# Optimization experiments

Measured on AMD Instinct MI355X. Metric: run time of the kernel, lower is better.

Reference implementation:

```python
import jax, jax.numpy as jnp
import numpy as np

NO, NR, E, D = 50000, 2000, 600000, 128
NEG_SLOPE = 0.2


def setup_inputs() -> dict:
    key = jax.random.key(0)
    ks = jax.random.split(key, 16)
    p = lambda k, shape: jax.random.normal(k, shape, dtype=jnp.float32) * 0.05
    return {
        "x_order": jax.random.normal(ks[0], (NO, D), dtype=jnp.float32),
        "x_rider": jax.random.normal(ks[1], (NR, D), dtype=jnp.float32),
        "order_idx": jax.random.randint(ks[2], (E,), 0, NO),
        "rider_idx": jax.random.randint(ks[3], (E,), 0, NR),
        # GATConv layer 1 (order_input_dim=128 -> hidden_dim=128, heads=1)
        "Ws1": p(ks[4], (D, D)), "Wd1": p(ks[5], (D, D)),
        "as1": p(ks[6], (D,)), "ad1": p(ks[7], (D,)), "b1": jnp.zeros((D,), jnp.float32),
        # GATConv layer 2 (hidden_dim=128 -> output_dim=128, heads=1)
        "Ws2": p(ks[8], (D, D)), "Wd2": p(ks[9], (D, D)),
        "as2": p(ks[10], (D,)), "ad2": p(ks[11], (D,)), "b2": jnp.zeros((D,), jnp.float32),
    }


def _segment_softmax(e, seg, num_segments):
    # numerically-stable softmax over edges grouped by destination node
    m = jax.ops.segment_max(e, seg, num_segments=num_segments)
    ex = jnp.exp(e - m[seg])
    s = jax.ops.segment_sum(ex, seg, num_segments=num_segments)
    return ex / (s[seg] + 1e-16)


def _gat_bipartite(x_src, x_dst, oi, ri, Ws, Wd, a_src, a_dst, b, n_dst):
    # PyG GATConv, heads=1, bipartite (src=order, dst=rider), no self-loops
    hs = x_src @ Ws            # [NO, D]
    hd = x_dst @ Wd            # [NR, D]
    alpha_s = hs @ a_src       # [NO]
    alpha_d = hd @ a_dst       # [NR]
    e = jax.nn.leaky_relu(alpha_s[oi] + alpha_d[ri], NEG_SLOPE)  # [E]
    alpha = _segment_softmax(e, ri, n_dst)                        # [E]
    out = jax.ops.segment_sum(alpha[:, None] * hs[oi], ri, num_segments=n_dst)
    return out + b


def reference(x_order, x_rider, order_idx, rider_idx,
              Ws1, Wd1, as1, ad1, b1, Ws2, Wd2, as2, ad2, b2):
    n_rider = x_rider.shape[0]
    # layer 1: update riders; order features pass through
    r1 = jax.nn.relu(_gat_bipartite(x_order, x_rider, order_idx, rider_idx,
                                    Ws1, Wd1, as1, ad1, b1, n_rider))
    o1 = jax.nn.relu(x_order)
    # layer 2
    r2 = _gat_bipartite(o1, r1, order_idx, rider_idx,
                        Ws2, Wd2, as2, ad2, b2, n_rider)
    # per-edge gather-dot-sigmoid scoring
    scores = jnp.sum(o1[order_idx] * r2[rider_idx], axis=1)
    return jax.nn.sigmoid(scores)
```

## Files before the change

kernel.cpp:

```cpp
#include <hip/hip_runtime.h>
#include <hip/hip_fp16.h>
#include <math.h>

#define NO 50000
#define NR 2000
#define NE 600000
#define D  128
#define NEG_SLOPE 0.2f
#define CAP 448
#define SLOT 512
#define NB 256
#define CH ((NE + NB - 1) / NB)

__global__ void prep_hist(const int* __restrict__ ri, int* __restrict__ blockHist,
                          const float* __restrict__ Ws1, const float* __restrict__ as1,
                          const float* __restrict__ Wd1, const float* __restrict__ ad1,
                          const float* __restrict__ Ws2, const float* __restrict__ as2,
                          const float* __restrict__ Wd2, const float* __restrict__ ad2,
                          float* __restrict__ wsv1, float* __restrict__ wdv1,
                          float* __restrict__ wsv2, float* __restrict__ wdv2) {
    __shared__ int h[NR];
    int t = threadIdx.x;
    if (blockIdx.x < NB) {
        int b = blockIdx.x;
        for (int i = t; i < NR; i += 256) h[i] = 0;
        __syncthreads();
        int lo = b * CH;
        int hi = lo + CH; if (hi > NE) hi = NE;
        for (int i = lo + t; i < hi; i += 256) atomicAdd(&h[ri[i]], 1);
        __syncthreads();
        for (int i = t; i < NR; i += 256) blockHist[(size_t)b * NR + i] = h[i];
    } else if (t < 128) {
        int k = t;
        float s1 = 0.f, d1 = 0.f, s2 = 0.f, d2 = 0.f;
        for (int j = 0; j < D; ++j) {
            s1 += Ws1[k * D + j] * as1[j];
            d1 += Wd1[k * D + j] * ad1[j];
            s2 += Ws2[k * D + j] * as2[j];
            d2 += Wd2[k * D + j] * ad2[j];
        }
        wsv1[k] = s1; wdv1[k] = d1; wsv2[k] = s2; wdv2[k] = d2;
    }
}

__global__ void prep_scan(const float* __restrict__ x, const float* __restrict__ xr,
                          const float* __restrict__ wsv1, const float* __restrict__ wsv2,
                          const float* __restrict__ wdv1,
                          float* __restrict__ as1o, float* __restrict__ as2o,
                          float* __restrict__ ad1r, __half* __restrict__ x16,
                          int* __restrict__ blockHist, int* __restrict__ total) {
    int lane = threadIdx.x & 63;
    int b = blockIdx.x;
    if (b < NO / 4) {
        int row = b * 4 + (threadIdx.x >> 6);
        float2 xv = ((const float2*)(x + (size_t)row * D))[lane];
        float2 w1 = ((const float2*)wsv1)[lane];
        float2 w2 = ((const float2*)wsv2)[lane];
        float rx0 = fmaxf(xv.x, 0.f), rx1 = fmaxf(xv.y, 0.f);
        ((__half2*)(x16 + (size_t)row * D))[lane] = __floats2half2_rn(xv.x, xv.y);
        float a1 = xv.x * w1.x + xv.y * w1.y;
        float a2 = rx0 * w2.x + rx1 * w2.y;
        for (int off = 32; off; off >>= 1) {
            a1 += __shfl_down(a1, off);
            a2 += __shfl_down(a2, off);
        }
        if (lane == 0) { as1o[row] = a1; as2o[row] = a2; }
    } else if (b < NO / 4 + NR / 4) {
        int row = (b - NO / 4) * 4 + (threadIdx.x >> 6);
        float2 xv = ((const float2*)(xr + (size_t)row * D))[lane];
        float2 w1 = ((const float2*)wdv1)[lane];
        float a = xv.x * w1.x + xv.y * w1.y;
        for (int off = 32; off; off >>= 1) a += __shfl_down(a, off);
        if (lane == 0) ad1r[row] = a;
    } else {
        int v = b - (NO / 4 + NR / 4);
        int r = v * 4 + (threadIdx.x >> 6);
        if (r >= NR) return;
        int b0 = lane * 4;
        int v0 = blockHist[(size_t)(b0 + 0) * NR + r];
        int v1 = blockHist[(size_t)(b0 + 1) * NR + r];
        int v2 = blockHist[(size_t)(b0 + 2) * NR + r];
        int v3 = blockHist[(size_t)(b0 + 3) * NR + r];
        int s = v0 + v1 + v2 + v3;
        int incl = s;
        for (int off = 1; off < 64; off <<= 1) {
            int u = __shfl_up(incl, off);
            if (lane >= off) incl += u;
        }
        int base = incl - s;
        blockHist[(size_t)(b0 + 0) * NR + r] = base;
        blockHist[(size_t)(b0 + 1) * NR + r] = base + v0;
        blockHist[(size_t)(b0 + 2) * NR + r] = base + v0 + v1;
        blockHist[(size_t)(b0 + 3) * NR + r] = base + v0 + v1 + v2;
        int tot = __shfl(incl, 63);
        if (lane == 0) total[r] = tot;
    }
}

__global__ void scatter_kernel(const int* __restrict__ oi, const int* __restrict__ ri,
                               const int* __restrict__ blockHist,
                               int2* __restrict__ sOE) {
    __shared__ int h[NR];
    int b = blockIdx.x, t = threadIdx.x;
    for (int i = t; i < NR; i += 256) h[i] = 0;
    __syncthreads();
    int lo = b * CH;
    int hi = lo + CH; if (hi > NE) hi = NE;
    for (int i = lo + t; i < hi; i += 256) {
        int r = ri[i];
        int rank = atomicAdd(&h[r], 1);
        int pos = r * SLOT + blockHist[(size_t)b * NR + r] + rank;
        sOE[pos] = make_int2(oi[i], i);
    }
}

__global__ void __launch_bounds__(256)
agg12(const __half* __restrict__ x16,
      const float* __restrict__ as1o, const float* __restrict__ as2o,
      const float* __restrict__ ad1r,
      const int* __restrict__ cnt, const int2* __restrict__ sOE,
      const float* __restrict__ W1, const float* __restrict__ b1,
      const float* __restrict__ wdv2,
      const float* __restrict__ W2, const float* __restrict__ b2,
      float* __restrict__ out) {
    __shared__ int   sO[CAP];
    __shared__ int   sE[CAP];
    __shared__ float red[256];
    __shared__ float red8[256][9];
    __shared__ float tl[D];
    __shared__ float r2s[D];
    __shared__ float wred[4];
    int r = blockIdx.x, t = threadIdx.x;
    int base = r * SLOT, n = cnt[r];
    int grp = t >> 4, lh = t & 15;

    int lim = n < CAP ? n : CAP;
    for (int i = t; i < lim; i += 256) {
        int2 v = sOE[base + i];
        sO[i] = v.x; sE[i] = v.y;
    }
    float ad1 = ad1r[r];
    __syncthreads();

    float acc[8];
#pragma unroll
    for (int k = 0; k < 8; ++k) acc[k] = 0.f;
    float ls = 0.f;
    if (n <= CAP) {
        int i = grp;
        for (; i + 16 < n; i += 32) {
            int o0 = sO[i], o1 = sO[i + 16];
            uint4 h0 = ((const uint4*)(x16 + (size_t)o0 * D))[lh];
            uint4 h1 = ((const uint4*)(x16 + (size_t)o1 * D))[lh];
            float e0 = as1o[o0] + ad1;
            float e1 = as1o[o1] + ad1;
            e0 = (e0 > 0.f) ? e0 : NEG_SLOPE * e0;
            e1 = (e1 > 0.f) ? e1 : NEG_SLOPE * e1;
            float a0 = __expf(e0), a1 = __expf(e1);
            ls += a0 + a1;
            const __half2* p0 = (const __half2*)&h0;
            const __half2* p1 = (const __half2*)&h1;
#pragma unroll
            for (int q = 0; q < 4; ++q) {
                float2 f0 = __half22float2(p0[q]);
                float2 f1 = __half22float2(p1[q]);
                acc[2 * q]     += a0 * f0.x + a1 * f1.x;
                acc[2 * q + 1] += a0 * f0.y + a1 * f1.y;
            }
        }
        if (i < n) {
            int o0 = sO[i];
            uint4 h0 = ((const uint4*)(x16 + (size_t)o0 * D))[lh];
            float e0 = as1o[o0] + ad1;
            e0 = (e0 > 0.f) ? e0 : NEG_SLOPE * e0;
            float a0 = __expf(e0);
            ls += a0;
            const __half2* p0 = (const __half2*)&h0;
#pragma unroll
            for (int q = 0; q < 4; ++q) {
                float2 f0 = __half22float2(p0[q]);
                acc[2 * q]     += a0 * f0.x;
                acc[2 * q + 1] += a0 * f0.y;
            }
        }
    } else {
        for (int i = grp; i < n; i += 16) {
            int o0 = (i < CAP) ? sO[i] : sOE[base + i].x;
            uint4 h0 = ((const uint4*)(x16 + (size_t)o0 * D))[lh];
            float e0 = as1o[o0] + ad1;
            e0 = (e0 > 0.f) ? e0 : NEG_SLOPE * e0;
            float a0 = __expf(e0);
            ls += a0;
            const __half2* p0 = (const __half2*)&h0;
#pragma unroll
            for (int q = 0; q < 4; ++q) {
                float2 f0 = __half22float2(p0[q]);
                acc[2 * q]     += a0 * f0.x;
                acc[2 * q + 1] += a0 * f0.y;
            }
        }
    }
    {
        float lsv = (lh == 0) ? ls : 0.f;
        lsv += __shfl_down(lsv, 32);
        lsv += __shfl_down(lsv, 16);
        lsv += __shfl_down(lsv, 8);
        lsv += __shfl_down(lsv, 4);
        lsv += __shfl_down(lsv, 2);
        lsv += __shfl_down(lsv, 1);
        if ((t & 63) == 0) wred[t >> 6] = lsv;
#pragma unroll
        for (int k = 0; k < 8; ++k) red8[t][k] = acc[k];
    }
    __syncthreads();
    if (t < D) {
        int lh2 = t >> 3, k = t & 7;
        float s = 0.f;
#pragma unroll
        for (int g = 0; g < 16; ++g) s += red8[g * 16 + lh2][k];
        float inv1 = 1.f / (wred[0] + wred[1] + wred[2] + wred[3] + 1e-16f);
        tl[t] = s * inv1;
    }
    __syncthreads();

    {
        int d = t & 127, h = t >> 7;
        float a = 0.f;
        for (int k = h * 64; k < h * 64 + 64; ++k) a += tl[k] * W1[k * D + d];
        red[t] = a;
    }
    __syncthreads();
    {
        float v = 0.f;
        if (t < 128) v = fmaxf(red[t] + red[t + 128] + b1[t], 0.f) * wdv2[t];
        v += __shfl_down(v, 32);
        v += __shfl_down(v, 16);
        v += __shfl_down(v, 8);
        v += __shfl_down(v, 4);
        v += __shfl_down(v, 2);
        v += __shfl_down(v, 1);
        if ((t & 63) == 0) wred[t >> 6] = v;
    }
    __syncthreads();
    float ad2 = wred[0] + wred[1] + wred[2] + wred[3];
    __syncthreads();

#pragma unroll
    for (int k = 0; k < 8; ++k) acc[k] = 0.f;
    ls = 0.f;
    if (n <= CAP) {
        int i = grp;
        for (; i + 16 < n; i += 32) {
            int o0 = sO[i], o1 = sO[i + 16];
            uint4 h0 = ((const uint4*)(x16 + (size_t)o0 * D))[lh];
            uint4 h1 = ((const uint4*)(x16 + (size_t)o1 * D))[lh];
            float e0 = as2o[o0] + ad2;
            float e1 = as2o[o1] + ad2;
            e0 = (e0 > 0.f) ? e0 : NEG_SLOPE * e0;
            e1 = (e1 > 0.f) ? e1 : NEG_SLOPE * e1;
            float a0 = __expf(e0), a1 = __expf(e1);
            ls += a0 + a1;
            const __half2* p0 = (const __half2*)&h0;
            const __half2* p1 = (const __half2*)&h1;
#pragma unroll
            for (int q = 0; q < 4; ++q) {
                float2 f0 = __half22float2(p0[q]);
                float2 f1 = __half22float2(p1[q]);
                acc[2 * q]     += a0 * fmaxf(f0.x, 0.f) + a1 * fmaxf(f1.x, 0.f);
                acc[2 * q + 1] += a0 * fmaxf(f0.y, 0.f) + a1 * fmaxf(f1.y, 0.f);
            }
        }
        if (i < n) {
            int o0 = sO[i];
            uint4 h0 = ((const uint4*)(x16 + (size_t)o0 * D))[lh];
            float e0 = as2o[o0] + ad2;
            e0 = (e0 > 0.f) ? e0 : NEG_SLOPE * e0;
            float a0 = __expf(e0);
            ls += a0;
            const __half2* p0 = (const __half2*)&h0;
#pragma unroll
            for (int q = 0; q < 4; ++q) {
                float2 f0 = __half22float2(p0[q]);
                acc[2 * q]     += a0 * fmaxf(f0.x, 0.f);
                acc[2 * q + 1] += a0 * fmaxf(f0.y, 0.f);
            }
        }
    } else {
        for (int i = grp; i < n; i += 16) {
            int o0 = (i < CAP) ? sO[i] : sOE[base + i].x;
            uint4 h0 = ((const uint4*)(x16 + (size_t)o0 * D))[lh];
            float e0 = as2o[o0] + ad2;
            e0 = (e0 > 0.f) ? e0 : NEG_SLOPE * e0;
            float a0 = __expf(e0);
            ls += a0;
            const __half2* p0 = (const __half2*)&h0;
#pragma unroll
            for (int q = 0; q < 4; ++q) {
                float2 f0 = __half22float2(p0[q]);
                acc[2 * q]     += a0 * fmaxf(f0.x, 0.f);
                acc[2 * q + 1] += a0 * fmaxf(f0.y, 0.f);
            }
        }
    }
    {
        float lsv = (lh == 0) ? ls : 0.f;
        lsv += __shfl_down(lsv, 32);
        lsv += __shfl_down(lsv, 16);
        lsv += __shfl_down(lsv, 8);
        lsv += __shfl_down(lsv, 4);
        lsv += __shfl_down(lsv, 2);
        lsv += __shfl_down(lsv, 1);
        if ((t & 63) == 0) wred[t >> 6] = lsv;
#pragma unroll
        for (int k = 0; k < 8; ++k) red8[t][k] = acc[k];
    }
    __syncthreads();
    if (t < D) {
        int lh2 = t >> 3, k = t & 7;
        float s = 0.f;
#pragma unroll
        for (int g = 0; g < 16; ++g) s += red8[g * 16 + lh2][k];
        float inv2 = 1.f / (wred[0] + wred[1] + wred[2] + wred[3] + 1e-16f);
        tl[t] = s * inv2;
    }
    __syncthreads();

    {
        int d = t & 127, h = t >> 7;
        float a = 0.f;
        for (int k = h * 64; k < h * 64 + 64; ++k) a += tl[k] * W2[k * D + d];
        red[t] = a;
    }
    __syncthreads();
    if (t < 128) r2s[t] = red[t] + red[t + 128] + b2[t];
    __syncthreads();

    float r2v[8];
#pragma unroll
    for (int k = 0; k < 8; ++k) r2v[k] = r2s[lh * 8 + k];
    if (n <= CAP) {
        int i = grp;
        for (; i + 16 < n; i += 32) {
            int o0 = sO[i], o1 = sO[i + 16];
            int e0 = sE[i], e1 = sE[i + 16];
            uint4 h0 = ((const uint4*)(x16 + (size_t)o0 * D))[lh];
            uint4 h1 = ((const uint4*)(x16 + (size_t)o1 * D))[lh];
            const __half2* p0 = (const __half2*)&h0;
            const __half2* p1 = (const __half2*)&h1;
            float pa = 0.f, pb = 0.f;
#pragma unroll
            for (int q = 0; q < 4; ++q) {
                float2 f0 = __half22float2(p0[q]);
                float2 f1 = __half22float2(p1[q]);
                pa += fmaxf(f0.x, 0.f) * r2v[2 * q] + fmaxf(f0.y, 0.f) * r2v[2 * q + 1];
                pb += fmaxf(f1.x, 0.f) * r2v[2 * q] + fmaxf(f1.y, 0.f) * r2v[2 * q + 1];
            }
            pa += __shfl_xor(pa, 8); pb += __shfl_xor(pb, 8);
            pa += __shfl_xor(pa, 4); pb += __shfl_xor(pb, 4);
            pa += __shfl_xor(pa, 2); pb += __shfl_xor(pb, 2);
            pa += __shfl_xor(pa, 1); pb += __shfl_xor(pb, 1);
            if (lh == 0) {
                out[e0] = 1.f / (1.f + __expf(-pa));
                out[e1] = 1.f / (1.f + __expf(-pb));
            }
        }
        if (i < n) {
            int o0 = sO[i], e0 = sE[i];
            uint4 h0 = ((const uint4*)(x16 + (size_t)o0 * D))[lh];
            const __half2* p0 = (const __half2*)&h0;
            float pa = 0.f;
#pragma unroll
            for (int q = 0; q < 4; ++q) {
                float2 f0 = __half22float2(p0[q]);
                pa += fmaxf(f0.x, 0.f) * r2v[2 * q] + fmaxf(f0.y, 0.f) * r2v[2 * q + 1];
            }
            pa += __shfl_xor(pa, 8);
            pa += __shfl_xor(pa, 4);
            pa += __shfl_xor(pa, 2);
            pa += __shfl_xor(pa, 1);
            if (lh == 0) out[e0] = 1.f / (1.f + __expf(-pa));
        }
    } else {
        for (int i = grp; i < n; i += 16) {
            int o0, e0;
            if (i < CAP) { o0 = sO[i]; e0 = sE[i]; }
            else { int2 v = sOE[base + i]; o0 = v.x; e0 = v.y; }
            uint4 h0 = ((const uint4*)(x16 + (size_t)o0 * D))[lh];
            const __half2* p0 = (const __half2*)&h0;
            float pa = 0.f;
#pragma unroll
            for (int q = 0; q < 4; ++q) {
                float2 f0 = __half22float2(p0[q]);
                pa += fmaxf(f0.x, 0.f) * r2v[2 * q] + fmaxf(f0.y, 0.f) * r2v[2 * q + 1];
            }
            pa += __shfl_xor(pa, 8);
            pa += __shfl_xor(pa, 4);
            pa += __shfl_xor(pa, 2);
            pa += __shfl_xor(pa, 1);
            if (lh == 0) out[e0] = 1.f / (1.f + __expf(-pa));
        }
    }
}

extern "C" void kernel_launch(void* const* d_in, const int* in_sizes, int n_in,
                              void* d_out, int out_size, void* d_ws, size_t ws_size,
                              hipStream_t stream) {
    const float* x_order = (const float*)d_in[0];
    const float* x_rider = (const float*)d_in[1];
    const int*   oi      = (const int*)d_in[2];
    const int*   ri      = (const int*)d_in[3];
    const float* Ws1 = (const float*)d_in[4];
    const float* Wd1 = (const float*)d_in[5];
    const float* as1 = (const float*)d_in[6];
    const float* ad1 = (const float*)d_in[7];
    const float* b1  = (const float*)d_in[8];
    const float* Ws2 = (const float*)d_in[9];
    const float* Wd2 = (const float*)d_in[10];
    const float* as2 = (const float*)d_in[11];
    const float* ad2 = (const float*)d_in[12];
    const float* b2  = (const float*)d_in[13];
    float* out = (float*)d_out;

    char* w = (char*)d_ws;
    float* wsv1 = (float*)w; w += 512;
    float* wdv1 = (float*)w; w += 512;
    float* wsv2 = (float*)w; w += 512;
    float* wdv2 = (float*)w; w += 512;
    float* as1o = (float*)w; w += (size_t)NO * 4;
    float* as2o = (float*)w; w += (size_t)NO * 4;
    float* ad1r = (float*)w; w += (size_t)NR * 4;
    int* total  = (int*)w;   w += (size_t)NR * 4;
    int* blockHist = (int*)w; w += (size_t)NB * NR * 4;
    int2* sOE   = (int2*)w;  w += (size_t)NR * SLOT * 8;
    __half* x16 = (__half*)w; w += (size_t)NO * D * 2;

    prep_hist<<<NB + 1, 256, 0, stream>>>(ri, blockHist,
                                          Ws1, as1, Wd1, ad1, Ws2, as2, Wd2, ad2,
                                          wsv1, wdv1, wsv2, wdv2);
    prep_scan<<<NO / 4 + NR / 4 + 500, 256, 0, stream>>>(x_order, x_rider,
                                                         wsv1, wsv2, wdv1,
                                                         as1o, as2o, ad1r, x16,
                                                         blockHist, total);
    scatter_kernel<<<NB, 256, 0, stream>>>(oi, ri, blockHist, sOE);
    agg12<<<NR, 256, 0, stream>>>(x16, as1o, as2o, ad1r, total, sOE,
                                  Ws1, b1, wdv2, Ws2, b2, out);
}
```

Baseline: 214.5 us.

## Cache gathered order rows in LDS across passes and double agg block size

The first aggregation pass now stores each gathered fp16 order row and its layer-2 attention score in shared memory (up to CAP edges). Layer 2 and the scoring pass then read from LDS instead of re-gathering from global memory. The block grows to 512 threads, and the partial-sum reduction is reworked to use wave shuffles before a smaller shared buffer. The roughly 115KB LDS cache limits occupancy to about one block per CU, which may hurt latency hiding for the gathers.

```diff
diff --git a/kernel.cpp b/kernel.cpp
--- a/kernel.cpp
+++ b/kernel.cpp
@@ -114,7 +114,7 @@
     }
 }
 
-__global__ void __launch_bounds__(256)
+__global__ void __launch_bounds__(512)
 agg12(const __half* __restrict__ x16,
       const float* __restrict__ as1o, const float* __restrict__ as2o,
       const float* __restrict__ ad1r,
@@ -123,19 +123,22 @@
       const float* __restrict__ wdv2,
       const float* __restrict__ W2, const float* __restrict__ b2,
       float* __restrict__ out) {
+    __shared__ uint4 xc4[CAP * 16];
     __shared__ int   sO[CAP];
     __shared__ int   sE[CAP];
-    __shared__ float red[256];
-    __shared__ float red8[256][9];
+    __shared__ float sA2[CAP];
+    __shared__ float red[512];
+    __shared__ float red8s[128][9];
     __shared__ float tl[D];
     __shared__ float r2s[D];
-    __shared__ float wred[4];
+    __shared__ float wred[8];
     int r = blockIdx.x, t = threadIdx.x;
     int base = r * SLOT, n = cnt[r];
     int grp = t >> 4, lh = t & 15;
+    int wave = t >> 6;
 
     int lim = n < CAP ? n : CAP;
-    for (int i = t; i < lim; i += 256) {
+    for (int i = t; i < lim; i += 512) {
         int2 v = sOE[base + i];
         sO[i] = v.x; sE[i] = v.y;
     }
@@ -148,16 +151,20 @@
     float ls = 0.f;
     if (n <= CAP) {
         int i = grp;
-        for (; i + 16 < n; i += 32) {
-            int o0 = sO[i], o1 = sO[i + 16];
+        for (; i + 32 < n; i += 64) {
+            int o0 = sO[i], o1 = sO[i + 32];
             uint4 h0 = ((const uint4*)(x16 + (size_t)o0 * D))[lh];
             uint4 h1 = ((const uint4*)(x16 + (size_t)o1 * D))[lh];
+            float s20 = as2o[o0], s21 = as2o[o1];
             float e0 = as1o[o0] + ad1;
             float e1 = as1o[o1] + ad1;
             e0 = (e0 > 0.f) ? e0 : NEG_SLOPE * e0;
             e1 = (e1 > 0.f) ? e1 : NEG_SLOPE * e1;
             float a0 = __expf(e0), a1 = __expf(e1);
             ls += a0 + a1;
+            xc4[i * 16 + lh] = h0;
+            xc4[(i + 32) * 16 + lh] = h1;
+            if (lh == 0) { sA2[i] = s20; sA2[i + 32] = s21; }
             const __half2* p0 = (const __half2*)&h0;
             const __half2* p1 = (const __half2*)&h1;
 #pragma unroll
@@ -171,10 +178,13 @@
         if (i < n) {
             int o0 = sO[i];
             uint4 h0 = ((const uint4*)(x16 + (size_t)o0 * D))[lh];
+            float s20 = as2o[o0];
             float e0 = as1o[o0] + ad1;
             e0 = (e0 > 0.f) ? e0 : NEG_SLOPE * e0;
             float a0 = __expf(e0);
             ls += a0;
+            xc4[i * 16 + lh] = h0;
+            if (lh == 0) sA2[i] = s20;
             const __half2* p0 = (const __half2*)&h0;
 #pragma unroll
             for (int q = 0; q < 4; ++q) {
@@ -184,13 +194,17 @@
             }
         }
     } else {
-        for (int i = grp; i < n; i += 16) {
+        for (int i = grp; i < n; i += 32) {
             int o0 = (i < CAP) ? sO[i] : sOE[base + i].x;
             uint4 h0 = ((const uint4*)(x16 + (size_t)o0 * D))[lh];
             float e0 = as1o[o0] + ad1;
             e0 = (e0 > 0.f) ? e0 : NEG_SLOPE * e0;
             float a0 = __expf(e0);
             ls += a0;
+            if (i < CAP) {
+                xc4[i * 16 + lh] = h0;
+                if (lh == 0) sA2[i] = as2o[o0];
+            }
             const __half2* p0 = (const __half2*)&h0;
 #pragma unroll
             for (int q = 0; q < 4; ++q) {
@@ -208,17 +222,24 @@
         lsv += __shfl_down(lsv, 4);
         lsv += __shfl_down(lsv, 2);
         lsv += __shfl_down(lsv, 1);
-        if ((t & 63) == 0) wred[t >> 6] = lsv;
-#pragma unroll
-        for (int k = 0; k < 8; ++k) red8[t][k] = acc[k];
+        if ((t & 63) == 0) wred[wave] = lsv;
+#pragma unroll
+        for (int k = 0; k < 8; ++k) acc[k] += __shfl_down(acc[k], 16);
+#pragma unroll
+        for (int k = 0; k < 8; ++k) acc[k] += __shfl_down(acc[k], 32);
+        if ((t & 63) < 16) {
+#pragma unroll
+            for (int k = 0; k < 8; ++k) red8s[wave * 16 + lh][k] = acc[k];
+        }
     }
     __syncthreads();
     if (t < D) {
         int lh2 = t >> 3, k = t & 7;
         float s = 0.f;
 #pragma unroll
-        for (int g = 0; g < 16; ++g) s += red8[g * 16 + lh2][k];
-        float inv1 = 1.f / (wred[0] + wred[1] + wred[2] + wred[3] + 1e-16f);
+        for (int w = 0; w < 8; ++w) s += red8s[w * 16 + lh2][k];
+        float inv1 = 1.f / (wred[0] + wred[1] + wred[2] + wred[3] +
+                            wred[4] + wred[5] + wred[6] + wred[7] + 1e-16f);
         tl[t] = s * inv1;
     }
     __syncthreads();
@@ -226,23 +247,25 @@
     {
         int d = t & 127, h = t >> 7;
         float a = 0.f;
-        for (int k = h * 64; k < h * 64 + 64; ++k) a += tl[k] * W1[k * D + d];
+        for (int k = h * 32; k < h * 32 + 32; ++k) a += tl[k] * W1[k * D + d];
         red[t] = a;
     }
     __syncthreads();
     {
         float v = 0.f;
-        if (t < 128) v = fmaxf(red[t] + red[t + 128] + b1[t], 0.f) * wdv2[t];
+        if (t < 128) v = fmaxf(red[t] + red[t + 128] + red[t + 256] + red[t + 384]
+                               + b1[t], 0.f) * wdv2[t];
         v += __shfl_down(v, 32);
         v += __shfl_down(v, 16);
         v += __shfl_down(v, 8);
         v += __shfl_down(v, 4);
         v += __shfl_down(v, 2);
         v += __shfl_down(v, 1);
-        if ((t & 63) == 0) wred[t >> 6] = v;
-    }
-    __syncthreads();
-    float ad2 = wred[0] + wred[1] + wred[2] + wred[3];
+        if ((t & 63) == 0) wred[wave] = v;
+    }
+    __syncthreads();
+    float ad2 = wred[0] + wred[1] + wred[2] + wred[3] +
+                wred[4] + wred[5] + wred[6] + wred[7];
     __syncthreads();
 
 #pragma unroll
@@ -250,12 +273,11 @@
     ls = 0.f;
     if (n <= CAP) {
         int i = grp;
-        for (; i + 16 < n; i += 32) {
-            int o0 = sO[i], o1 = sO[i + 16];
-            uint4 h0 = ((const uint4*)(x16 + (size_t)o0 * D))[lh];
-            uint4 h1 = ((const uint4*)(x16 + (size_t)o1 * D))[lh];
-            float e0 = as2o[o0] + ad2;
-            float e1 = as2o[o1] + ad2;
+        for (; i + 32 < n; i += 64) {
+            uint4 h0 = xc4[i * 16 + lh];
+            uint4 h1 = xc4[(i + 32) * 16 + lh];
+            float e0 = sA2[i] + ad2;
+            float e1 = sA2[i + 32] + ad2;
             e0 = (e0 > 0.f) ? e0 : NEG_SLOPE * e0;
             e1 = (e1 > 0.f) ? e1 : NEG_SLOPE * e1;
             float a0 = __expf(e0), a1 = __expf(e1);
@@ -271,9 +293,8 @@
             }
         }
         if (i < n) {
-            int o0 = sO[i];
-            uint4 h0 = ((const uint4*)(x16 + (size_t)o0 * D))[lh];
-            float e0 = as2o[o0] + ad2;
+            uint4 h0 = xc4[i * 16 + lh];
+            float e0 = sA2[i] + ad2;
             e0 = (e0 > 0.f) ? e0 : NEG_SLOPE * e0;
             float a0 = __expf(e0);
             ls += a0;
@@ -286,10 +307,15 @@
             }
         }
     } else {
-        for (int i = grp; i < n; i += 16) {
-            int o0 = (i < CAP) ? sO[i] : sOE[base + i].x;
-            uint4 h0 = ((const uint4*)(x16 + (size_t)o0 * D))[lh];
-            float e0 = as2o[o0] + ad2;
+        for (int i = grp; i < n; i += 32) {
+            uint4 h0; float s2;
+            if (i < CAP) { h0 = xc4[i * 16 + lh]; s2 = sA2[i]; }
+            else {
+                int o0 = sOE[base + i].x;
+                h0 = ((const uint4*)(x16 + (size_t)o0 * D))[lh];
+                s2 = as2o[o0];
+            }
+            float e0 = s2 + ad2;
             e0 = (e0 > 0.f) ? e0 : NEG_SLOPE * e0;
             float a0 = __expf(e0);
             ls += a0;
@@ -310,17 +336,24 @@
         lsv += __shfl_down(lsv, 4);
         lsv += __shfl_down(lsv, 2);
         lsv += __shfl_down(lsv, 1);
-        if ((t & 63) == 0) wred[t >> 6] = lsv;
-#pragma unroll
-        for (int k = 0; k < 8; ++k) red8[t][k] = acc[k];
+        if ((t & 63) == 0) wred[wave] = lsv;
+#pragma unroll
+        for (int k = 0; k < 8; ++k) acc[k] += __shfl_down(acc[k], 16);
+#pragma unroll
+        for (int k = 0; k < 8; ++k) acc[k] += __shfl_down(acc[k], 32);
+        if ((t & 63) < 16) {
+#pragma unroll
+            for (int k = 0; k < 8; ++k) red8s[wave * 16 + lh][k] = acc[k];
+        }
     }
     __syncthreads();
     if (t < D) {
         int lh2 = t >> 3, k = t & 7;
         float s = 0.f;
 #pragma unroll
-        for (int g = 0; g < 16; ++g) s += red8[g * 16 + lh2][k];
-        float inv2 = 1.f / (wred[0] + wred[1] + wred[2] + wred[3] + 1e-16f);
+        for (int w = 0; w < 8; ++w) s += red8s[w * 16 + lh2][k];
+        float inv2 = 1.f / (wred[0] + wred[1] + wred[2] + wred[3] +
+                            wred[4] + wred[5] + wred[6] + wred[7] + 1e-16f);
         tl[t] = s * inv2;
     }
     __syncthreads();
@@ -328,11 +361,11 @@
     {
         int d = t & 127, h = t >> 7;
         float a = 0.f;
-        for (int k = h * 64; k < h * 64 + 64; ++k) a += tl[k] * W2[k * D + d];
+        for (int k = h * 32; k < h * 32 + 32; ++k) a += tl[k] * W2[k * D + d];
         red[t] = a;
     }
     __syncthreads();
-    if (t < 128) r2s[t] = red[t] + red[t + 128] + b2[t];
+    if (t < 128) r2s[t] = red[t] + red[t + 128] + red[t + 256] + red[t + 384] + b2[t];
     __syncthreads();
 
     float r2v[8];
@@ -340,11 +373,10 @@
     for (int k = 0; k < 8; ++k) r2v[k] = r2s[lh * 8 + k];
     if (n <= CAP) {
         int i = grp;
-        for (; i + 16 < n; i += 32) {
-            int o0 = sO[i], o1 = sO[i + 16];
-            int e0 = sE[i], e1 = sE[i + 16];
-            uint4 h0 = ((const uint4*)(x16 + (size_t)o0 * D))[lh];
-            uint4 h1 = ((const uint4*)(x16 + (size_t)o1 * D))[lh];
+        for (; i + 32 < n; i += 64) {
+            uint4 h0 = xc4[i * 16 + lh];
+            uint4 h1 = xc4[(i + 32) * 16 + lh];
+            int e0 = sE[i], e1 = sE[i + 32];
             const __half2* p0 = (const __half2*)&h0;
             const __half2* p1 = (const __half2*)&h1;
             float pa = 0.f, pb = 0.f;
@@ -365,8 +397,8 @@
             }
         }
         if (i < n) {
-            int o0 = sO[i], e0 = sE[i];
-            uint4 h0 = ((const uint4*)(x16 + (size_t)o0 * D))[lh];
+            uint4 h0 = xc4[i * 16 + lh];
+            int e0 = sE[i];
             const __half2* p0 = (const __half2*)&h0;
             float pa = 0.f;
 #pragma unroll
@@ -381,11 +413,14 @@
             if (lh == 0) out[e0] = 1.f / (1.f + __expf(-pa));
         }
     } else {
-        for (int i = grp; i < n; i += 16) {
-            int o0, e0;
-            if (i < CAP) { o0 = sO[i]; e0 = sE[i]; }
-            else { int2 v = sOE[base + i]; o0 = v.x; e0 = v.y; }
-            uint4 h0 = ((const uint4*)(x16 + (size_t)o0 * D))[lh];
+        for (int i = grp; i < n; i += 32) {
+            uint4 h0; int e0;
+            if (i < CAP) { h0 = xc4[i * 16 + lh]; e0 = sE[i]; }
+            else {
+                int2 v = sOE[base + i];
+                h0 = ((const uint4*)(x16 + (size_t)v.x * D))[lh];
+                e0 = v.y;
+            }
             const __half2* p0 = (const __half2*)&h0;
             float pa = 0.f;
 #pragma unroll
@@ -442,6 +477,6 @@
                                                          as1o, as2o, ad1r, x16,
                                                          blockHist, total);
     scatter_kernel<<<NB, 256, 0, stream>>>(oi, ri, blockHist, sOE);
-    agg12<<<NR, 256, 0, stream>>>(x16, as1o, as2o, ad1r, total, sOE,
+    agg12<<<NR, 512, 0, stream>>>(x16, as1o, as2o, ad1r, total, sOE,
                                   Ws1, b1, wdv2, Ws2, b2, out);
 }
```

Result: slower. 237.4 us (+10.6%).

## Cache gathered order rows and layer-2 attention logits in LDS across passes

Applied to the files above, without the earlier changes.

During the first aggregation pass, each block stores the first CAPC gathered fp16 order rows and the as2o logits for its edges in shared memory. The second aggregation pass and the scoring pass then read these from LDS instead of re-gathering them from global memory. The cross-group partial-sum reduction also switches from a 256-row shared buffer to wave shuffles, which shrinks that buffer. The row cache takes about 70 KB of LDS per block, which may limit how many blocks fit on a CU and so reduce occupancy.

```diff
diff --git a/kernel.cpp b/kernel.cpp
--- a/kernel.cpp
+++ b/kernel.cpp
@@ -8,6 +8,7 @@
 #define D  128
 #define NEG_SLOPE 0.2f
 #define CAP 448
+#define CAPC 272
 #define SLOT 512
 #define NB 256
 #define CH ((NE + NB - 1) / NB)
@@ -123,16 +124,19 @@
       const float* __restrict__ wdv2,
       const float* __restrict__ W2, const float* __restrict__ b2,
       float* __restrict__ out) {
+    __shared__ uint4 xc4[CAPC * 16];
     __shared__ int   sO[CAP];
     __shared__ int   sE[CAP];
+    __shared__ float sA2[CAP];
     __shared__ float red[256];
-    __shared__ float red8[256][9];
+    __shared__ float red8s[64][9];
     __shared__ float tl[D];
     __shared__ float r2s[D];
     __shared__ float wred[4];
     int r = blockIdx.x, t = threadIdx.x;
     int base = r * SLOT, n = cnt[r];
     int grp = t >> 4, lh = t & 15;
+    int wave = t >> 6;
 
     int lim = n < CAP ? n : CAP;
     for (int i = t; i < lim; i += 256) {
@@ -152,12 +156,16 @@
             int o0 = sO[i], o1 = sO[i + 16];
             uint4 h0 = ((const uint4*)(x16 + (size_t)o0 * D))[lh];
             uint4 h1 = ((const uint4*)(x16 + (size_t)o1 * D))[lh];
+            float s20 = as2o[o0], s21 = as2o[o1];
             float e0 = as1o[o0] + ad1;
             float e1 = as1o[o1] + ad1;
             e0 = (e0 > 0.f) ? e0 : NEG_SLOPE * e0;
             e1 = (e1 > 0.f) ? e1 : NEG_SLOPE * e1;
             float a0 = __expf(e0), a1 = __expf(e1);
             ls += a0 + a1;
+            if (i < CAPC)      xc4[i * 16 + lh] = h0;
+            if (i + 16 < CAPC) xc4[(i + 16) * 16 + lh] = h1;
+            if (lh == 0) { sA2[i] = s20; sA2[i + 16] = s21; }
             const __half2* p0 = (const __half2*)&h0;
             const __half2* p1 = (const __half2*)&h1;
 #pragma unroll
@@ -171,10 +179,13 @@
         if (i < n) {
             int o0 = sO[i];
             uint4 h0 = ((const uint4*)(x16 + (size_t)o0 * D))[lh];
+            float s20 = as2o[o0];
             float e0 = as1o[o0] + ad1;
             e0 = (e0 > 0.f) ? e0 : NEG_SLOPE * e0;
             float a0 = __expf(e0);
             ls += a0;
+            if (i < CAPC) xc4[i * 16 + lh] = h0;
+            if (lh == 0) sA2[i] = s20;
             const __half2* p0 = (const __half2*)&h0;
 #pragma unroll
             for (int q = 0; q < 4; ++q) {
@@ -191,6 +202,8 @@
             e0 = (e0 > 0.f) ? e0 : NEG_SLOPE * e0;
             float a0 = __expf(e0);
             ls += a0;
+            if (i < CAPC) xc4[i * 16 + lh] = h0;
+            if (i < CAP && lh == 0) sA2[i] = as2o[o0];
             const __half2* p0 = (const __half2*)&h0;
 #pragma unroll
             for (int q = 0; q < 4; ++q) {
@@ -208,16 +221,22 @@
         lsv += __shfl_down(lsv, 4);
         lsv += __shfl_down(lsv, 2);
         lsv += __shfl_down(lsv, 1);
-        if ((t & 63) == 0) wred[t >> 6] = lsv;
-#pragma unroll
-        for (int k = 0; k < 8; ++k) red8[t][k] = acc[k];
+        if ((t & 63) == 0) wred[wave] = lsv;
+#pragma unroll
+        for (int k = 0; k < 8; ++k) acc[k] += __shfl_down(acc[k], 16);
+#pragma unroll
+        for (int k = 0; k < 8; ++k) acc[k] += __shfl_down(acc[k], 32);
+        if ((t & 63) < 16) {
+#pragma unroll
+            for (int k = 0; k < 8; ++k) red8s[wave * 16 + lh][k] = acc[k];
+        }
     }
     __syncthreads();
     if (t < D) {
         int lh2 = t >> 3, k = t & 7;
         float s = 0.f;
 #pragma unroll
-        for (int g = 0; g < 16; ++g) s += red8[g * 16 + lh2][k];
+        for (int w = 0; w < 4; ++w) s += red8s[w * 16 + lh2][k];
         float inv1 = 1.f / (wred[0] + wred[1] + wred[2] + wred[3] + 1e-16f);
         tl[t] = s * inv1;
     }
@@ -239,7 +258,7 @@
         v += __shfl_down(v, 4);
         v += __shfl_down(v, 2);
         v += __shfl_down(v, 1);
-        if ((t & 63) == 0) wred[t >> 6] = v;
+        if ((t & 63) == 0) wred[wave] = v;
     }
     __syncthreads();
     float ad2 = wred[0] + wred[1] + wred[2] + wred[3];
@@ -251,11 +270,12 @@
     if (n <= CAP) {
         int i = grp;
         for (; i + 16 < n; i += 32) {
-            int o0 = sO[i], o1 = sO[i + 16];
-            uint4 h0 = ((const uint4*)(x16 + (size_t)o0 * D))[lh];
-            uint4 h1 = ((const uint4*)(x16 + (size_t)o1 * D))[lh];
-            float e0 = as2o[o0] + ad2;
-            float e1 = as2o[o1] + ad2;
+            uint4 h0 = (i < CAPC) ? xc4[i * 16 + lh]
+                       : ((const uint4*)(x16 + (size_t)sO[i] * D))[lh];
+            uint4 h1 = (i + 16 < CAPC) ? xc4[(i + 16) * 16 + lh]
+                       : ((const uint4*)(x16 + (size_t)sO[i + 16] * D))[lh];
+            float e0 = sA2[i] + ad2;
+            float e1 = sA2[i + 16] + ad2;
             e0 = (e0 > 0.f) ? e0 : NEG_SLOPE * e0;
             e1 = (e1 > 0.f) ? e1 : NEG_SLOPE * e1;
             float a0 = __expf(e0), a1 = __expf(e1);
@@ -271,9 +291,9 @@
             }
         }
         if (i < n) {
-            int o0 = sO[i];
-            uint4 h0 = ((const uint4*)(x16 + (size_t)o0 * D))[lh];
-            float e0 = as2o[o0] + ad2;
+            uint4 h0 = (i < CAPC) ? xc4[i * 16 + lh]
+                       : ((const uint4*)(x16 + (size_t)sO[i] * D))[lh];
+            float e0 = sA2[i] + ad2;
             e0 = (e0 > 0.f) ? e0 : NEG_SLOPE * e0;
             float a0 = __expf(e0);
             ls += a0;
@@ -287,9 +307,14 @@
         }
     } else {
         for (int i = grp; i < n; i += 16) {
-            int o0 = (i < CAP) ? sO[i] : sOE[base + i].x;
-            uint4 h0 = ((const uint4*)(x16 + (size_t)o0 * D))[lh];
-            float e0 = as2o[o0] + ad2;
+            uint4 h0; float s2;
+            if (i < CAPC) { h0 = xc4[i * 16 + lh]; s2 = sA2[i]; }
+            else {
+                int o0 = (i < CAP) ? sO[i] : sOE[base + i].x;
+                h0 = ((const uint4*)(x16 + (size_t)o0 * D))[lh];
+                s2 = (i < CAP) ? sA2[i] : as2o[o0];
+            }
+            float e0 = s2 + ad2;
             e0 = (e0 > 0.f) ? e0 : NEG_SLOPE * e0;
             float a0 = __expf(e0);
             ls += a0;
@@ -310,16 +335,22 @@
         lsv += __shfl_down(lsv, 4);
         lsv += __shfl_down(lsv, 2);
         lsv += __shfl_down(lsv, 1);
-        if ((t & 63) == 0) wred[t >> 6] = lsv;
-#pragma unroll
-        for (int k = 0; k < 8; ++k) red8[t][k] = acc[k];
+        if ((t & 63) == 0) wred[wave] = lsv;
+#pragma unroll
+        for (int k = 0; k < 8; ++k) acc[k] += __shfl_down(acc[k], 16);
+#pragma unroll
+        for (int k = 0; k < 8; ++k) acc[k] += __shfl_down(acc[k], 32);
+        if ((t & 63) < 16) {
+#pragma unroll
+            for (int k = 0; k < 8; ++k) red8s[wave * 16 + lh][k] = acc[k];
+        }
     }
     __syncthreads();
     if (t < D) {
         int lh2 = t >> 3, k = t & 7;
         float s = 0.f;
 #pragma unroll
-        for (int g = 0; g < 16; ++g) s += red8[g * 16 + lh2][k];
+        for (int w = 0; w < 4; ++w) s += red8s[w * 16 + lh2][k];
         float inv2 = 1.f / (wred[0] + wred[1] + wred[2] + wred[3] + 1e-16f);
         tl[t] = s * inv2;
     }
@@ -341,10 +372,11 @@
     if (n <= CAP) {
         int i = grp;
         for (; i + 16 < n; i += 32) {
-            int o0 = sO[i], o1 = sO[i + 16];
+            uint4 h0 = (i < CAPC) ? xc4[i * 16 + lh]
+                       : ((const uint4*)(x16 + (size_t)sO[i] * D))[lh];
+            uint4 h1 = (i + 16 < CAPC) ? xc4[(i + 16) * 16 + lh]
+                       : ((const uint4*)(x16 + (size_t)sO[i + 16] * D))[lh];
             int e0 = sE[i], e1 = sE[i + 16];
-            uint4 h0 = ((const uint4*)(x16 + (size_t)o0 * D))[lh];
-            uint4 h1 = ((const uint4*)(x16 + (size_t)o1 * D))[lh];
             const __half2* p0 = (const __half2*)&h0;
             const __half2* p1 = (const __half2*)&h1;
             float pa = 0.f, pb = 0.f;
@@ -365,8 +397,9 @@
             }
         }
         if (i < n) {
-            int o0 = sO[i], e0 = sE[i];
-            uint4 h0 = ((const uint4*)(x16 + (size_t)o0 * D))[lh];
+            uint4 h0 = (i < CAPC) ? xc4[i * 16 + lh]
+                       : ((const uint4*)(x16 + (size_t)sO[i] * D))[lh];
+            int e0 = sE[i];
             const __half2* p0 = (const __half2*)&h0;
             float pa = 0.f;
 #pragma unroll
@@ -382,10 +415,14 @@
         }
     } else {
         for (int i = grp; i < n; i += 16) {
-            int o0, e0;
-            if (i < CAP) { o0 = sO[i]; e0 = sE[i]; }
-            else { int2 v = sOE[base + i]; o0 = v.x; e0 = v.y; }
-            uint4 h0 = ((const uint4*)(x16 + (size_t)o0 * D))[lh];
+            uint4 h0; int e0;
+            if (i < CAPC) { h0 = xc4[i * 16 + lh]; e0 = sE[i]; }
+            else {
+                int o0; 
+                if (i < CAP) { o0 = sO[i]; e0 = sE[i]; }
+                else { int2 v = sOE[base + i]; o0 = v.x; e0 = v.y; }
+                h0 = ((const uint4*)(x16 + (size_t)o0 * D))[lh];
+            }
             const __half2* p0 = (const __half2*)&h0;
             float pa = 0.f;
 #pragma unroll
```

Result: slower. 225.7 us (+5.2%).

## Replace histogram-scan-scatter bucketing with global atomic counters fused into prep

Applied to the files above, without the earlier changes.

Edges are bucketed by rider using a global atomicAdd on a per-rider counter, done inside the prep kernel. This replaces the per-block histogram, prefix scan and separate scatter kernel. It removes one launch, the block histogram buffer and its scan pass. In exchange, edge order within each bucket becomes nondeterministic, and global atomics contend on 2000 counters.

```diff
diff --git a/kernel.cpp b/kernel.cpp
--- a/kernel.cpp
+++ b/kernel.cpp
@@ -9,27 +9,18 @@
 #define NEG_SLOPE 0.2f
 #define CAP 448
 #define SLOT 512
-#define NB 256
-#define CH ((NE + NB - 1) / NB)
-
-__global__ void prep_hist(const int* __restrict__ ri, int* __restrict__ blockHist,
+#define SCB 2048
+
+__global__ void prep_init(int* __restrict__ cnt,
                           const float* __restrict__ Ws1, const float* __restrict__ as1,
                           const float* __restrict__ Wd1, const float* __restrict__ ad1,
                           const float* __restrict__ Ws2, const float* __restrict__ as2,
                           const float* __restrict__ Wd2, const float* __restrict__ ad2,
                           float* __restrict__ wsv1, float* __restrict__ wdv1,
                           float* __restrict__ wsv2, float* __restrict__ wdv2) {
-    __shared__ int h[NR];
     int t = threadIdx.x;
-    if (blockIdx.x < NB) {
-        int b = blockIdx.x;
-        for (int i = t; i < NR; i += 256) h[i] = 0;
-        __syncthreads();
-        int lo = b * CH;
-        int hi = lo + CH; if (hi > NE) hi = NE;
-        for (int i = lo + t; i < hi; i += 256) atomicAdd(&h[ri[i]], 1);
-        __syncthreads();
-        for (int i = t; i < NR; i += 256) blockHist[(size_t)b * NR + i] = h[i];
+    if (blockIdx.x == 0) {
+        for (int i = t; i < NR; i += 256) cnt[i] = 0;
     } else if (t < 128) {
         int k = t;
         float s1 = 0.f, d1 = 0.f, s2 = 0.f, d2 = 0.f;
@@ -48,7 +39,8 @@
                           const float* __restrict__ wdv1,
                           float* __restrict__ as1o, float* __restrict__ as2o,
                           float* __restrict__ ad1r, __half* __restrict__ x16,
-                          int* __restrict__ blockHist, int* __restrict__ total) {
+                          const int* __restrict__ oi, const int* __restrict__ ri,
+                          int* __restrict__ cnt, int2* __restrict__ sOE) {
     int lane = threadIdx.x & 63;
     int b = blockIdx.x;
     if (b < NO / 4) {
@@ -74,43 +66,12 @@
         if (lane == 0) ad1r[row] = a;
     } else {
         int v = b - (NO / 4 + NR / 4);
-        int r = v * 4 + (threadIdx.x >> 6);
-        if (r >= NR) return;
-        int b0 = lane * 4;
-        int v0 = blockHist[(size_t)(b0 + 0) * NR + r];
-        int v1 = blockHist[(size_t)(b0 + 1) * NR + r];
-        int v2 = blockHist[(size_t)(b0 + 2) * NR + r];
-        int v3 = blockHist[(size_t)(b0 + 3) * NR + r];
-        int s = v0 + v1 + v2 + v3;
-        int incl = s;
-        for (int off = 1; off < 64; off <<= 1) {
-            int u = __shfl_up(incl, off);
-            if (lane >= off) incl += u;
-        }
-        int base = incl - s;
-        blockHist[(size_t)(b0 + 0) * NR + r] = base;
-        blockHist[(size_t)(b0 + 1) * NR + r] = base + v0;
-        blockHist[(size_t)(b0 + 2) * NR + r] = base + v0 + v1;
-        blockHist[(size_t)(b0 + 3) * NR + r] = base + v0 + v1 + v2;
-        int tot = __shfl(incl, 63);
-        if (lane == 0) total[r] = tot;
-    }
-}
-
-__global__ void scatter_kernel(const int* __restrict__ oi, const int* __restrict__ ri,
-                               const int* __restrict__ blockHist,
-                               int2* __restrict__ sOE) {
-    __shared__ int h[NR];
-    int b = blockIdx.x, t = threadIdx.x;
-    for (int i = t; i < NR; i += 256) h[i] = 0;
-    __syncthreads();
-    int lo = b * CH;
-    int hi = lo + CH; if (hi > NE) hi = NE;
-    for (int i = lo + t; i < hi; i += 256) {
-        int r = ri[i];
-        int rank = atomicAdd(&h[r], 1);
-        int pos = r * SLOT + blockHist[(size_t)b * NR + r] + rank;
-        sOE[pos] = make_int2(oi[i], i);
+        int gid = v * 256 + threadIdx.x;
+        for (int e = gid; e < NE; e += SCB * 256) {
+            int r = ri[e];
+            int pos = atomicAdd(&cnt[r], 1);
+            sOE[(size_t)r * SLOT + pos] = make_int2(oi[e], e);
+        }
     }
 }
 
@@ -429,19 +390,17 @@
     float* as1o = (float*)w; w += (size_t)NO * 4;
     float* as2o = (float*)w; w += (size_t)NO * 4;
     float* ad1r = (float*)w; w += (size_t)NR * 4;
-    int* total  = (int*)w;   w += (size_t)NR * 4;
-    int* blockHist = (int*)w; w += (size_t)NB * NR * 4;
+    int* cnt    = (int*)w;   w += (size_t)NR * 4;
     int2* sOE   = (int2*)w;  w += (size_t)NR * SLOT * 8;
     __half* x16 = (__half*)w; w += (size_t)NO * D * 2;
 
-    prep_hist<<<NB + 1, 256, 0, stream>>>(ri, blockHist,
-                                          Ws1, as1, Wd1, ad1, Ws2, as2, Wd2, ad2,
-                                          wsv1, wdv1, wsv2, wdv2);
-    prep_scan<<<NO / 4 + NR / 4 + 500, 256, 0, stream>>>(x_order, x_rider,
+    prep_init<<<2, 256, 0, stream>>>(cnt,
+                                     Ws1, as1, Wd1, ad1, Ws2, as2, Wd2, ad2,
+                                     wsv1, wdv1, wsv2, wdv2);
+    prep_scan<<<NO / 4 + NR / 4 + SCB, 256, 0, stream>>>(x_order, x_rider,
                                                          wsv1, wsv2, wdv1,
                                                          as1o, as2o, ad1r, x16,
-                                                         blockHist, total);
-    scatter_kernel<<<NB, 256, 0, stream>>>(oi, ri, blockHist, sOE);
-    agg12<<<NR, 256, 0, stream>>>(x16, as1o, as2o, ad1r, total, sOE,
+                                                         oi, ri, cnt, sOE);
+    agg12<<<NR, 256, 0, stream>>>(x16, as1o, as2o, ad1r, cnt, sOE,
                                   Ws1, b1, wdv2, Ws2, b2, out);
 }
```

Result: slower. 265.4 us (+23.7%).
